# Optimization experiments

Measured on AMD Instinct MI355X. Metric: run time of the kernel, lower is better.

Reference implementation:

```python
import jax, jax.numpy as jnp
import numpy as np

B, N, C_IN, L, C_OUT = 8, 50000, 32, 9, 64
M, NNZ = 12500, 37500


def setup_inputs() -> dict:
    key = jax.random.key(0)
    k = jax.random.split(key, 7)
    x = jax.random.normal(k[0], (B, N, C_IN), dtype=jnp.float32)
    weight = jax.random.normal(k[1], (L * C_IN, C_OUT), dtype=jnp.float32) * (1.0 / np.sqrt(L * C_IN))
    bias = jax.random.normal(k[2], (C_OUT,), dtype=jnp.float32) * 0.01
    values = jax.random.uniform(k[3], (NNZ,), dtype=jnp.float32)
    spiral_indices = jax.random.randint(k[4], (N, L), 0, N, dtype=jnp.int64)
    rows = jax.random.randint(k[5], (NNZ,), 0, M, dtype=jnp.int64)
    cols = jax.random.randint(k[6], (NNZ,), 0, N, dtype=jnp.int64)
    return {"x": x, "weight": weight, "bias": bias, "values": values,
            "spiral_indices": spiral_indices, "rows": rows, "cols": cols,
            "num_out_verts": M}


def reference(x, weight, bias, values, spiral_indices, rows, cols, num_out_verts):
    b, n, c = x.shape
    # SpiralConv: gather spiral neighborhoods, flatten, linear
    g = x[:, spiral_indices]                      # [B, N, L, C]
    g = g.reshape(b, n, -1)                       # [B, N, L*C]
    out = jnp.einsum('bnk,ko->bno', g, weight) + bias
    out = jax.nn.elu(out)                         # [B, N, C_OUT]
    # Pool: sparse down_transform (gather, scale, scatter_add)
    gathered = out[:, cols] * values[None, :, None]          # [B, NNZ, C_OUT]
    pooled = jnp.zeros((b, num_out_verts, out.shape[-1]), dtype=out.dtype)
    pooled = pooled.at[:, rows].add(gathered)                # [B, M, C_OUT]
    return pooled
```

## Files before the change

### kernel.cpp

```cpp
#include <hip/hip_runtime.h>

#define BATCH   8
#define NVERT   50000
#define CIN     32
#define LSP     9
#define KDIM    288
#define COUT    64
#define MVERT   12500
#define NNZ     37500

#define TILE_T  64
#define TPB     586
#define PADK    296
#define NFRAG   2304

typedef __attribute__((ext_vector_type(8))) short  short8;
typedef __attribute__((ext_vector_type(4))) float  floatx4;

static __device__ __forceinline__ unsigned short f2bf(float f) {
    union { float f; unsigned int u; } c; c.f = f;
    unsigned int u = c.u;
    return (unsigned short)((u + 0x7fffu + ((u >> 16) & 1u)) >> 16);
}

__global__ void pack_w_kernel(const float* __restrict__ w, unsigned short* __restrict__ wp) {
    int f = blockIdx.x * blockDim.x + threadIdx.x;
    if (f >= NFRAG) return;
    int s    = f >> 8;
    int g    = (f >> 6) & 3;
    int lane = f & 63;
    int quad = lane >> 4, n = lane & 15;
    int k0   = s * 32 + quad * 8;
    int col  = g * 16 + n;
    unsigned short tmp[8];
    #pragma unroll
    for (int j = 0; j < 8; ++j)
        tmp[j] = f2bf(w[(size_t)(k0 + j) * COUT + col]);
    ((uint4*)wp)[f] = *(uint4*)tmp;
}

__global__ __launch_bounds__(256)
void spiral_mfma_kernel(const float* __restrict__ x,
                        const unsigned short* __restrict__ wp,
                        const float* __restrict__ bias,
                        const float* __restrict__ vals,
                        const int* __restrict__ spiral,
                        const int* __restrict__ rows,
                        const int* __restrict__ cols,
                        float* __restrict__ out)
{
    __shared__ unsigned short sG[TILE_T * PADK];

    const int bid  = blockIdx.x;
    const int b    = bid / TPB;
    const int tile = bid - b * TPB;
    const int z0   = tile * TILE_T;
    const int tcnt = min(TILE_T, NNZ - z0);
    const int tid  = threadIdx.x;

    const float* xb = x + (size_t)b * NVERT * CIN;

    #pragma unroll
    for (int i = 0; i < 9; ++i) {
        int u   = tid + i * 256;
        int t   = u / 36;
        int rem = u - t * 36;
        int r   = rem >> 2;
        int q   = rem & 3;
        int z   = z0 + t; if (z >= NNZ) z = NNZ - 1;
        int col = cols[z];
        int idx = spiral[col * LSP + r];
        const float4* src = (const float4*)(xb + (size_t)idx * CIN + q * 8);
        float4 a = src[0], c = src[1];
        unsigned short tmp[8];
        tmp[0] = f2bf(a.x); tmp[1] = f2bf(a.y); tmp[2] = f2bf(a.z); tmp[3] = f2bf(a.w);
        tmp[4] = f2bf(c.x); tmp[5] = f2bf(c.y); tmp[6] = f2bf(c.z); tmp[7] = f2bf(c.w);
        *(uint4*)(&sG[t * PADK + r * 32 + q * 8]) = *(uint4*)tmp;
    }
    __syncthreads();

    const int wv   = tid >> 6;
    const int lane = tid & 63;
    const int quad = lane >> 4;
    const int m16  = lane & 15;

    const unsigned short* aptr = &sG[(16 * wv + m16) * PADK + quad * 8];

    floatx4 acc[4];
    #pragma unroll
    for (int g = 0; g < 4; ++g) acc[g] = (floatx4){0.f, 0.f, 0.f, 0.f};

    #pragma unroll
    for (int s = 0; s < 9; ++s) {
        short8 af = *(const short8*)(aptr + s * 32);
        #pragma unroll
        for (int g = 0; g < 4; ++g) {
            short8 bf = *(const short8*)(wp + ((size_t)((s * 4 + g) * 64 + lane)) * 8);
            acc[g] = __builtin_amdgcn_mfma_f32_16x16x32_bf16(af, bf, acc[g], 0, 0, 0);
        }
    }

    #pragma unroll
    for (int r = 0; r < 4; ++r) {
        int t = 16 * wv + quad * 4 + r;
        if (t < tcnt) {
            int z     = z0 + t;
            float v   = vals[z];
            int row   = rows[z];
            float* dst = out + ((size_t)b * MVERT + row) * COUT;
            #pragma unroll
            for (int g = 0; g < 4; ++g) {
                int ch  = g * 16 + m16;
                float y = acc[g][r] + bias[ch];
                y = (y > 0.0f) ? y : (__expf(y) - 1.0f);
                atomicAdd(dst + ch, y * v);
            }
        }
    }
}

extern "C" void kernel_launch(void* const* d_in, const int* in_sizes, int n_in,
                              void* d_out, int out_size, void* d_ws, size_t ws_size,
                              hipStream_t stream) {
    const float* x      = (const float*)d_in[0];
    const float* w      = (const float*)d_in[1];
    const float* bias   = (const float*)d_in[2];
    const float* vals   = (const float*)d_in[3];
    const int*   spiral = (const int*)d_in[4];
    const int*   rows   = (const int*)d_in[5];
    const int*   cols   = (const int*)d_in[6];
    float* out = (float*)d_out;
    unsigned short* wp = (unsigned short*)d_ws;

    hipMemsetAsync(d_out, 0, (size_t)out_size * sizeof(float), stream);
    pack_w_kernel<<<9, 256, 0, stream>>>(w, wp);
    spiral_mfma_kernel<<<BATCH * TPB, 256, 0, stream>>>(x, wp, bias, vals,
                                                        spiral, rows, cols, out);
}
```

Measured before the change: 196.5 us.

## Pre-convert x to bf16 and gather spiral rows via direct global-to-LDS DMA

A new prep kernel converts all of x to bf16 in the workspace, packs the weights and zeroes the output in one launch. This replaces the memset and the separate pack kernel. The main kernel then gathers neighbour rows from the bf16 copy with global_load_lds 16-byte DMAs straight into shared memory, laid out in MFMA fragment order. That removes per-element conversion and register staging from the gather and halves the gathered bytes. The cost is a full extra read and write of x (about 51 MB fp32 read, 26 MB bf16 written) every call.

```diff
diff --git a/kernel.cpp b/kernel.cpp
--- a/kernel.cpp
+++ b/kernel.cpp
@@ -1,18 +1,23 @@
 #include <hip/hip_runtime.h>
+#include <hip/hip_bf16.h>
 
 #define BATCH   8
 #define NVERT   50000
 #define CIN     32
 #define LSP     9
-#define KDIM    288
 #define COUT    64
 #define MVERT   12500
 #define NNZ     37500
 
 #define TILE_T  64
 #define TPB     586
-#define PADK    296
 #define NFRAG   2304
+#define XELEMS  (BATCH * NVERT * CIN)
+#define OUTDW   (BATCH * MVERT * COUT)
+
+#define PRE_BLOCKS  6250
+#define PACK_BLOCKS 9
+#define ZERO_BLOCKS 6250
 
 typedef __attribute__((ext_vector_type(8))) short  short8;
 typedef __attribute__((ext_vector_type(4))) float  floatx4;
@@ -23,33 +28,58 @@
     return (unsigned short)((u + 0x7fffu + ((u >> 16) & 1u)) >> 16);
 }
 
-__global__ void pack_w_kernel(const float* __restrict__ w, unsigned short* __restrict__ wp) {
-    int f = blockIdx.x * blockDim.x + threadIdx.x;
-    if (f >= NFRAG) return;
-    int s    = f >> 8;
-    int g    = (f >> 6) & 3;
-    int lane = f & 63;
-    int quad = lane >> 4, n = lane & 15;
-    int k0   = s * 32 + quad * 8;
-    int col  = g * 16 + n;
-    unsigned short tmp[8];
-    #pragma unroll
-    for (int j = 0; j < 8; ++j)
-        tmp[j] = f2bf(w[(size_t)(k0 + j) * COUT + col]);
-    ((uint4*)wp)[f] = *(uint4*)tmp;
+static __device__ __forceinline__ void dma16(const void* g, void* l) {
+    typedef __attribute__((address_space(1))) const void gvoid;
+    typedef __attribute__((address_space(3))) void lvoid;
+    __builtin_amdgcn_global_load_lds(
+        (gvoid*)(unsigned long long)g,
+        (lvoid*)(unsigned int)(unsigned long long)l,
+        16, 0, 0);
 }
 
 __global__ __launch_bounds__(256)
-void spiral_mfma_kernel(const float* __restrict__ x,
-                        const unsigned short* __restrict__ wp,
-                        const float* __restrict__ bias,
-                        const float* __restrict__ vals,
-                        const int* __restrict__ spiral,
-                        const int* __restrict__ rows,
-                        const int* __restrict__ cols,
-                        float* __restrict__ out)
+void prep_kernel(const float* __restrict__ x, const float* __restrict__ w,
+                 unsigned short* __restrict__ x16, unsigned short* __restrict__ wp,
+                 float* __restrict__ out)
 {
-    __shared__ unsigned short sG[TILE_T * PADK];
+    const int blk = blockIdx.x;
+    const int tid = threadIdx.x;
+    if (blk < PRE_BLOCKS) {
+        const size_t base = ((size_t)blk * 256 + tid) * 8;
+        const float4* s = (const float4*)(x + base);
+        float4 a = s[0], c = s[1];
+        unsigned short t[8];
+        t[0]=f2bf(a.x); t[1]=f2bf(a.y); t[2]=f2bf(a.z); t[3]=f2bf(a.w);
+        t[4]=f2bf(c.x); t[5]=f2bf(c.y); t[6]=f2bf(c.z); t[7]=f2bf(c.w);
+        *(uint4*)(x16 + base) = *(uint4*)t;
+    } else if (blk < PRE_BLOCKS + PACK_BLOCKS) {
+        const int f = (blk - PRE_BLOCKS) * 256 + tid;
+        if (f < NFRAG) {
+            int s = f >> 8, g = (f >> 6) & 3, lane = f & 63;
+            int k0 = s * 32 + (lane >> 4) * 8, col = g * 16 + (lane & 15);
+            unsigned short t[8];
+            #pragma unroll
+            for (int j = 0; j < 8; ++j)
+                t[j] = f2bf(w[(size_t)(k0 + j) * COUT + col]);
+            ((uint4*)wp)[f] = *(uint4*)t;
+        }
+    } else {
+        const size_t base = ((size_t)(blk - PRE_BLOCKS - PACK_BLOCKS) * 256 + tid) * 4;
+        if (base < OUTDW) *(uint4*)(out + base) = (uint4){0, 0, 0, 0};
+    }
+}
+
+__global__ __launch_bounds__(256)
+void spiral_mfma2_kernel(const unsigned short* __restrict__ x16,
+                         const unsigned short* __restrict__ wp,
+                         const float* __restrict__ bias,
+                         const float* __restrict__ vals,
+                         const int* __restrict__ spiral,
+                         const int* __restrict__ rows,
+                         const int* __restrict__ cols,
+                         float* __restrict__ out)
+{
+    __shared__ unsigned short sG[NFRAG * 8];
 
     const int bid  = blockIdx.x;
     const int b    = bid / TPB;
@@ -57,34 +87,26 @@
     const int z0   = tile * TILE_T;
     const int tcnt = min(TILE_T, NNZ - z0);
     const int tid  = threadIdx.x;
+    const int w    = tid >> 6;
+    const int lane = tid & 63;
 
-    const float* xb = x + (size_t)b * NVERT * CIN;
+    int zc = z0 + lane; if (zc >= NNZ) zc = NNZ - 1;
+    const int  c  = cols[zc];
+    const int* sp = spiral + c * LSP;
+    int idx[9];
+    #pragma unroll
+    for (int j = 0; j < 9; ++j) idx[j] = sp[j];
 
+    const unsigned short* xb = x16 + (size_t)b * NVERT * CIN;
     #pragma unroll
-    for (int i = 0; i < 9; ++i) {
-        int u   = tid + i * 256;
-        int t   = u / 36;
-        int rem = u - t * 36;
-        int r   = rem >> 2;
-        int q   = rem & 3;
-        int z   = z0 + t; if (z >= NNZ) z = NNZ - 1;
-        int col = cols[z];
-        int idx = spiral[col * LSP + r];
-        const float4* src = (const float4*)(xb + (size_t)idx * CIN + q * 8);
-        float4 a = src[0], c = src[1];
-        unsigned short tmp[8];
-        tmp[0] = f2bf(a.x); tmp[1] = f2bf(a.y); tmp[2] = f2bf(a.z); tmp[3] = f2bf(a.w);
-        tmp[4] = f2bf(c.x); tmp[5] = f2bf(c.y); tmp[6] = f2bf(c.z); tmp[7] = f2bf(c.w);
-        *(uint4*)(&sG[t * PADK + r * 32 + q * 8]) = *(uint4*)tmp;
+    for (int j = 0; j < 9; ++j) {
+        const unsigned short* src = xb + (size_t)idx[j] * CIN + w * 8;
+        dma16(src, sG + (size_t)(4 * j + w) * 512);
     }
     __syncthreads();
 
-    const int wv   = tid >> 6;
-    const int lane = tid & 63;
     const int quad = lane >> 4;
     const int m16  = lane & 15;
-
-    const unsigned short* aptr = &sG[(16 * wv + m16) * PADK + quad * 8];
 
     floatx4 acc[4];
     #pragma unroll
@@ -92,21 +114,21 @@
 
     #pragma unroll
     for (int s = 0; s < 9; ++s) {
-        short8 af = *(const short8*)(aptr + s * 32);
+        short8 af = *(const short8*)(sG + (size_t)((s * 4 + quad) * 64 + 16 * w + m16) * 8);
         #pragma unroll
         for (int g = 0; g < 4; ++g) {
-            short8 bf = *(const short8*)(wp + ((size_t)((s * 4 + g) * 64 + lane)) * 8);
+            short8 bf = *(const short8*)(wp + (size_t)((s * 4 + g) * 64 + lane) * 8);
             acc[g] = __builtin_amdgcn_mfma_f32_16x16x32_bf16(af, bf, acc[g], 0, 0, 0);
         }
     }
 
     #pragma unroll
     for (int r = 0; r < 4; ++r) {
-        int t = 16 * wv + quad * 4 + r;
+        int t = 16 * w + quad * 4 + r;
         if (t < tcnt) {
-            int z     = z0 + t;
-            float v   = vals[z];
-            int row   = rows[z];
+            int z   = z0 + t;
+            float v = vals[z];
+            int row = rows[z];
             float* dst = out + ((size_t)b * MVERT + row) * COUT;
             #pragma unroll
             for (int g = 0; g < 4; ++g) {
@@ -130,10 +152,12 @@
     const int*   rows   = (const int*)d_in[5];
     const int*   cols   = (const int*)d_in[6];
     float* out = (float*)d_out;
-    unsigned short* wp = (unsigned short*)d_ws;
 
-    hipMemsetAsync(d_out, 0, (size_t)out_size * sizeof(float), stream);
-    pack_w_kernel<<<9, 256, 0, stream>>>(w, wp);
-    spiral_mfma_kernel<<<BATCH * TPB, 256, 0, stream>>>(x, wp, bias, vals,
-                                                        spiral, rows, cols, out);
+    unsigned short* wp  = (unsigned short*)d_ws;
+    unsigned short* x16 = (unsigned short*)((char*)d_ws + (size_t)NFRAG * 16);
+
+    const int prep_grid = PRE_BLOCKS + PACK_BLOCKS + ZERO_BLOCKS;
+    prep_kernel<<<prep_grid, 256, 0, stream>>>(x, w, x16, wp, out);
+    spiral_mfma2_kernel<<<BATCH * TPB, 256, 0, stream>>>(x16, wp, bias, vals,
+                                                         spiral, rows, cols, out);
 }
```

New measurement: 211.2 us. 7.5% more time.
